# Kernel tuning notes

Hardware: AMD Instinct MI355X
Metric: run time of the kernel (lower is better)

Reference implementation:

```python
import jax, jax.numpy as jnp
import numpy as np

B, N, H = 4, 256, 256
BN_EPS = 1e-5
ETA_EPS = 1e-20


def setup_inputs() -> dict:
    key = jax.random.key(0)
    k1, k2, k3, k4 = jax.random.split(key, 4)
    scale = 1.0 / np.sqrt(H)
    return {
        "nodes_features": jax.random.normal(k1, (B, N, H), dtype=jnp.float32),
        "edges_features": jax.random.normal(k2, (B, N, N, H), dtype=jnp.float32),
        "W1": jax.random.normal(k3, (H, H), dtype=jnp.float32) * scale,
        "W2": jax.random.normal(k4, (H, H), dtype=jnp.float32) * scale,
        "gamma": jnp.ones((H,), dtype=jnp.float32),
        "beta": jnp.zeros((H,), dtype=jnp.float32),
    }


def reference(nodes_features, edges_features, W1, W2, gamma, beta):
    # Linear projections (nn.Linear: y = x @ W.T, no bias)
    x_left = jnp.einsum('bnh,oh->bno', nodes_features, W1)       # (B,N,H)
    x_w2 = jnp.einsum('bnh,oh->bno', nodes_features, W2)         # (B,N,H)

    # Edge gating: sigmoid-normalize over neighbor axis j (dim=2)
    sig = jax.nn.sigmoid(edges_features)                         # (B,N,N,H)
    eta = sig / (jnp.sum(sig, axis=2, keepdims=True) + ETA_EPS)  # (B,N,N,H)

    # Weighted aggregation: sum_j eta[b,i,j,h] * x_w2[b,j,h]
    right = jnp.einsum('bijh,bjh->bih', eta, x_w2)               # (B,N,H)

    equ = x_left + right                                         # (B,N,H)

    # BatchNorm1d over channel H with batch stats over (B, N) (training mode,
    # track_running_stats=False -> always uses batch statistics, biased var)
    mean = jnp.mean(equ, axis=(0, 1))                            # (H,)
    var = jnp.var(equ, axis=(0, 1))                              # (H,) biased
    normed = (equ - mean) * jax.lax.rsqrt(var + BN_EPS)
    return normed * gamma + beta
```

## Files before the change

kernel.cpp:

```cpp
#include <hip/hip_runtime.h>
#include <cstddef>

#define BB 4
#define NN 256
#define HH 256
#define BN_EPS 1e-5f
#define ETA_EPS 1e-20f

typedef float f4 __attribute__((ext_vector_type(4)));

__device__ __forceinline__ float fast_sigmoid(float x) {
    float ex = __expf(-x);
    return __builtin_amdgcn_rcpf(1.f + ex);
}

__global__ __launch_bounds__(256) void transpose_kernel(
    const float* __restrict__ W1, const float* __restrict__ W2,
    float* __restrict__ WT1, float* __restrict__ WT2,
    float* __restrict__ Ssum, float* __restrict__ Qsum)
{
    if (blockIdx.x == 32) {
        Ssum[threadIdx.x] = 0.f;
        Qsum[threadIdx.x] = 0.f;
        return;
    }
    const int which = blockIdx.x >> 4;
    const int tile  = blockIdx.x & 15;
    const int tr = (tile >> 2) << 6, tc = (tile & 3) << 6;
    const float* __restrict__ W  = which ? W2 : W1;
    float* __restrict__ WT       = which ? WT2 : WT1;

    __shared__ float tl[64][65];
    const int c = threadIdx.x & 63, p0 = threadIdx.x >> 6;
#pragma unroll
    for (int p = 0; p < 16; ++p) {
        int r = p * 4 + p0;
        tl[c][r] = W[(tr + r) * HH + tc + c];
    }
    __syncthreads();
#pragma unroll
    for (int p = 0; p < 16; ++p) {
        int cc = p * 4 + p0;
        WT[(tc + cc) * HH + tr + c] = tl[cc][c];
    }
}

__global__ __launch_bounds__(256) void proj_kernel(
    const float* __restrict__ nodes, const float* __restrict__ WT1,
    const float* __restrict__ WT2, float* __restrict__ xleft,
    float* __restrict__ xw2)
{
    const int wg    = blockIdx.x >> 2;
    const int which = (blockIdx.x >> 1) & 1;
    const int oh    = blockIdx.x & 1;
    const float* __restrict__ WT = which ? WT2 : WT1;
    float* __restrict__ dst      = which ? xw2 : xleft;
    const int t = threadIdx.x;

    __shared__ float xs[8][HH];
    {
        f4* xs4 = reinterpret_cast<f4*>(xs);
        const f4* nodes4 = reinterpret_cast<const f4*>(nodes) + wg * 512;
        xs4[t]       = nodes4[t];
        xs4[t + 256] = nodes4[t + 256];
    }
    __syncthreads();

    const int oq = t & 31;
    const int hg = t >> 5;
    const f4* __restrict__ WT4 = reinterpret_cast<const f4*>(WT);

    f4 acc[8];
#pragma unroll
    for (int r = 0; r < 8; ++r) acc[r] = (f4){0.f, 0.f, 0.f, 0.f};

    for (int hh = 0; hh < 32; ++hh) {
        const int h = hg * 32 + hh;
        f4 wv = WT4[h * 64 + oh * 32 + oq];
#pragma unroll
        for (int r = 0; r < 8; ++r)
            acc[r] += xs[r][h] * wv;
    }

    __shared__ f4 ps[8][8][32];
#pragma unroll
    for (int r = 0; r < 8; ++r) ps[hg][r][oq] = acc[r];
    __syncthreads();

    {
        const int r = t >> 5, o = t & 31;
        f4 v = (f4){0.f, 0.f, 0.f, 0.f};
#pragma unroll
        for (int g = 0; g < 8; ++g) v += ps[g][r][o];
        reinterpret_cast<f4*>(dst)[(wg * 8 + r) * 64 + oh * 32 + o] = v;
    }
}

__global__ __launch_bounds__(1024) void edge_kernel(
    const float* __restrict__ edges, const float* __restrict__ xw2,
    const float* __restrict__ xleft, float* __restrict__ equ,
    float* __restrict__ Ssum, float* __restrict__ Qsum)
{
    const int blk = blockIdx.x;
    const int ig  = blk >> 2;
    const int hs4 = (blk & 3) * 16;
    const int bi0 = ig * 8;
    const int b   = bi0 >> 8;
    const int t   = threadIdx.x;

    __shared__ f4 xw_s[NN][16];

    const f4* __restrict__ xw4 =
        reinterpret_cast<const f4*>(xw2) + (size_t)b * NN * 64;
#pragma unroll
    for (int m = 0; m < 4; ++m) {
        int idx = m * 1024 + t;
        int j = idx >> 4, q = idx & 15;
        xw_s[j][q] = xw4[j * 64 + hs4 + q];
    }
    __syncthreads();

    const int q  = t & 15;
    const int il = (t >> 4) & 7;
    const int jg = t >> 7;

    const f4* __restrict__ erow =
        reinterpret_cast<const f4*>(edges) +
        (size_t)(bi0 + il) * (NN * 64) + hs4 + q;

    float s0[4] = {0.f, 0.f, 0.f, 0.f};
    float s1[4] = {0.f, 0.f, 0.f, 0.f};

#pragma unroll 2
    for (int j = jg; j < NN; j += 8) {
        f4 e  = erow[j * 64];
        f4 xw = xw_s[j][q];
#pragma unroll
        for (int k = 0; k < 4; ++k) {
            float sg = fast_sigmoid(e[k]);
            s0[k] += sg;
            s1[k] += sg * xw[k];
        }
    }
    __syncthreads();

    float* red = reinterpret_cast<float*>(xw_s);
    {
        float* r0 = red + ((jg * 8 + il) * 16 + q) * 4;
        float* r1 = r0 + 4096;
#pragma unroll
        for (int k = 0; k < 4; ++k) { r0[k] = s0[k]; r1[k] = s1[k]; }
    }
    __syncthreads();

    float* st = red + 8192;

    if (t < 512) {
        const int il2 = t >> 6;
        const int ch  = t & 63;
        float S0 = 0.f, S1 = 0.f;
#pragma unroll
        for (int g = 0; g < 8; ++g) {
            S0 += red[(g * 8 + il2) * 64 + ch];
            S1 += red[(g * 8 + il2) * 64 + ch + 4096];
        }
        const size_t off = (size_t)(bi0 + il2) * HH + hs4 * 4 + ch;
        float ov = xleft[off] + S1 / (S0 + ETA_EPS);
        equ[off] = ov;
        st[(il2 * 64 + ch) * 2]     = ov;
        st[(il2 * 64 + ch) * 2 + 1] = ov * ov;
    }
    __syncthreads();

    if (t < 64) {
        float S = 0.f, Q = 0.f;
#pragma unroll
        for (int g = 0; g < 8; ++g) {
            S += st[(g * 64 + t) * 2];
            Q += st[(g * 64 + t) * 2 + 1];
        }
        atomicAdd(&Ssum[hs4 * 4 + t], S);
        atomicAdd(&Qsum[hs4 * 4 + t], Q);
    }
}

__global__ __launch_bounds__(256) void norm_kernel(
    const float* __restrict__ equ, const float* __restrict__ Ssum,
    const float* __restrict__ Qsum, const float* __restrict__ gamma,
    const float* __restrict__ beta, float* __restrict__ out)
{
    const int idx = blockIdx.x * 256 + threadIdx.x;
    const int c4  = idx & 63;
    f4 e = reinterpret_cast<const f4*>(equ)[idx];
    f4 S = reinterpret_cast<const f4*>(Ssum)[c4];
    f4 Q = reinterpret_cast<const f4*>(Qsum)[c4];
    f4 g = reinterpret_cast<const f4*>(gamma)[c4];
    f4 b = reinterpret_cast<const f4*>(beta)[c4];

    const float inv_n = 1.f / (float)(BB * NN);
    f4 o;
#pragma unroll
    for (int k = 0; k < 4; ++k) {
        float mean = S[k] * inv_n;
        float var  = Q[k] * inv_n - mean * mean;
        float rstd = rsqrtf(var + BN_EPS);
        o[k] = (e[k] - mean) * rstd * g[k] + b[k];
    }
    reinterpret_cast<f4*>(out)[idx] = o;
}

extern "C" void kernel_launch(void* const* d_in, const int* in_sizes, int n_in,
                              void* d_out, int out_size, void* d_ws, size_t ws_size,
                              hipStream_t stream) {
    (void)in_sizes; (void)n_in; (void)out_size; (void)ws_size;

    const float* nodes = (const float*)d_in[0];
    const float* edges = (const float*)d_in[1];
    const float* W1    = (const float*)d_in[2];
    const float* W2    = (const float*)d_in[3];
    const float* gamma = (const float*)d_in[4];
    const float* beta  = (const float*)d_in[5];
    float* out = (float*)d_out;

    const int nBN_H = BB * NN * HH;
    float* ws    = (float*)d_ws;
    float* xleft = ws;
    float* xw2   = ws + nBN_H;
    float* equ   = ws + 2 * nBN_H;
    float* WT1   = ws + 3 * nBN_H;
    float* WT2   = WT1 + HH * HH;
    float* Ssum  = WT2 + HH * HH;
    float* Qsum  = Ssum + HH;

    transpose_kernel<<<33, 256, 0, stream>>>(W1, W2, WT1, WT2, Ssum, Qsum);
    proj_kernel<<<512, 256, 0, stream>>>(nodes, WT1, WT2, xleft, xw2);
    edge_kernel<<<512, 1024, 0, stream>>>(edges, xw2, xleft, equ, Ssum, Qsum);
    norm_kernel<<<256, 256, 0, stream>>>(equ, Ssum, Qsum, gamma, beta, out);
}
```

Measured before the change: 63.14 us.

## Fuse weight transpose into projection kernel via double-buffered LDS staging

```diff
diff --git a/kernel.cpp b/kernel.cpp
--- a/kernel.cpp
+++ b/kernel.cpp
@@ -14,86 +14,69 @@
     return __builtin_amdgcn_rcpf(1.f + ex);
 }
 
-__global__ __launch_bounds__(256) void transpose_kernel(
-    const float* __restrict__ W1, const float* __restrict__ W2,
-    float* __restrict__ WT1, float* __restrict__ WT2,
-    float* __restrict__ Ssum, float* __restrict__ Qsum)
+__global__ __launch_bounds__(256) void proj_kernel(
+    const float* __restrict__ nodes, const float* __restrict__ W1,
+    const float* __restrict__ W2, float* __restrict__ xleft,
+    float* __restrict__ xw2, float* __restrict__ Ssum,
+    float* __restrict__ Qsum)
 {
-    if (blockIdx.x == 32) {
+    if (blockIdx.x == 512) {
         Ssum[threadIdx.x] = 0.f;
         Qsum[threadIdx.x] = 0.f;
         return;
     }
-    const int which = blockIdx.x >> 4;
-    const int tile  = blockIdx.x & 15;
-    const int tr = (tile >> 2) << 6, tc = (tile & 3) << 6;
-    const float* __restrict__ W  = which ? W2 : W1;
-    float* __restrict__ WT       = which ? WT2 : WT1;
-
-    __shared__ float tl[64][65];
-    const int c = threadIdx.x & 63, p0 = threadIdx.x >> 6;
-#pragma unroll
-    for (int p = 0; p < 16; ++p) {
-        int r = p * 4 + p0;
-        tl[c][r] = W[(tr + r) * HH + tc + c];
-    }
-    __syncthreads();
-#pragma unroll
-    for (int p = 0; p < 16; ++p) {
-        int cc = p * 4 + p0;
-        WT[(tc + cc) * HH + tr + c] = tl[cc][c];
-    }
-}
-
-__global__ __launch_bounds__(256) void proj_kernel(
-    const float* __restrict__ nodes, const float* __restrict__ WT1,
-    const float* __restrict__ WT2, float* __restrict__ xleft,
-    float* __restrict__ xw2)
-{
     const int wg    = blockIdx.x >> 2;
     const int which = (blockIdx.x >> 1) & 1;
     const int oh    = blockIdx.x & 1;
-    const float* __restrict__ WT = which ? WT2 : WT1;
-    float* __restrict__ dst      = which ? xw2 : xleft;
+    const float* __restrict__ W = which ? W2 : W1;
+    float* __restrict__ dst     = which ? xw2 : xleft;
     const int t = threadIdx.x;
 
     __shared__ float xs[8][HH];
+    __shared__ float wt[2][32][128];
+
     {
         f4* xs4 = reinterpret_cast<f4*>(xs);
         const f4* nodes4 = reinterpret_cast<const f4*>(nodes) + wg * 512;
         xs4[t]       = nodes4[t];
         xs4[t + 256] = nodes4[t + 256];
     }
-    __syncthreads();
-
+
+    const int rg = t >> 5;
     const int oq = t & 31;
-    const int hg = t >> 5;
-    const f4* __restrict__ WT4 = reinterpret_cast<const f4*>(WT);
-
-    f4 acc[8];
-#pragma unroll
-    for (int r = 0; r < 8; ++r) acc[r] = (f4){0.f, 0.f, 0.f, 0.f};
-
-    for (int hh = 0; hh < 32; ++hh) {
-        const int h = hg * 32 + hh;
-        f4 wv = WT4[h * 64 + oh * 32 + oq];
-#pragma unroll
-        for (int r = 0; r < 8; ++r)
-            acc[r] += xs[r][h] * wv;
-    }
-
-    __shared__ f4 ps[8][8][32];
-#pragma unroll
-    for (int r = 0; r < 8; ++r) ps[hg][r][oq] = acc[r];
-    __syncthreads();
-
-    {
-        const int r = t >> 5, o = t & 31;
-        f4 v = (f4){0.f, 0.f, 0.f, 0.f};
-#pragma unroll
-        for (int g = 0; g < 8; ++g) v += ps[g][r][o];
-        reinterpret_cast<f4*>(dst)[(wg * 8 + r) * 64 + oh * 32 + o] = v;
-    }
+    const int lr = t >> 3;
+    const int lc = t & 7;
+    const f4* __restrict__ W4 = reinterpret_cast<const f4*>(W);
+
+#define STAGE(buf, h0)                                                        \
+    {                                                                         \
+        _Pragma("unroll")                                                     \
+        for (int m = 0; m < 4; ++m) {                                         \
+            int o = lr + m * 32;                                              \
+            f4 w = W4[(size_t)(oh * 128 + o) * 64 + ((h0) >> 2) + lc];        \
+            _Pragma("unroll")                                                 \
+            for (int k = 0; k < 4; ++k) wt[buf][lc * 4 + k][o] = w[k];        \
+        }                                                                     \
+    }
+
+    STAGE(0, 0);
+    __syncthreads();
+
+    f4 acc = (f4){0.f, 0.f, 0.f, 0.f};
+#pragma unroll
+    for (int tile = 0; tile < 8; ++tile) {
+        const int buf = tile & 1;
+        if (tile < 7) STAGE(buf ^ 1, (tile + 1) * 32);
+        const f4* wrow = reinterpret_cast<const f4*>(wt[buf]);
+        const float* xr = &xs[rg][tile * 32];
+#pragma unroll
+        for (int hh = 0; hh < 32; ++hh)
+            acc += xr[hh] * wrow[hh * 32 + oq];
+        __syncthreads();
+    }
+#undef STAGE
+
+    reinterpret_cast<f4*>(dst)[(wg * 8 + rg) * 64 + oh * 32 + oq] = acc;
 }
 
 __global__ __launch_bounds__(1024) void edge_kernel(
@@ -227,13 +210,10 @@
     float* xleft = ws;
     float* xw2   = ws + nBN_H;
     float* equ   = ws + 2 * nBN_H;
-    float* WT1   = ws + 3 * nBN_H;
-    float* WT2   = WT1 + HH * HH;
-    float* Ssum  = WT2 + HH * HH;
+    float* Ssum  = ws + 3 * nBN_H;
     float* Qsum  = Ssum + HH;
 
-    transpose_kernel<<<33, 256, 0, stream>>>(W1, W2, WT1, WT2, Ssum, Qsum);
-    proj_kernel<<<512, 256, 0, stream>>>(nodes, WT1, WT2, xleft, xw2);
+    proj_kernel<<<513, 256, 0, stream>>>(nodes, W1, W2, xleft, xw2, Ssum, Qsum);
     edge_kernel<<<512, 1024, 0, stream>>>(edges, xw2, xleft, equ, Ssum, Qsum);
     norm_kernel<<<256, 256, 0, stream>>>(equ, Ssum, Qsum, gamma, beta, out);
 }
```

Result: slower. 68.53 us (+8.5%).
